# Performance work log

Measured on AMD Instinct MI355X. Metric: run time of the kernel, lower is better.

Reference implementation:

```python
import jax, jax.numpy as jnp
import numpy as np
from jax import lax

FEAT_STRIDE = 16
ANCHOR_DIMS = np.array([[64., 64.], [128., 128.], [256., 256.], [512., 512.]], np.float32)
A = ANCHOR_DIMS.shape[0]
SCALE = 1.0
PRE_NMS = 6000
POST_NMS = 300
NMS_THRESH = 0.7
MIN_SIZE = 16.0


def _anchors(H, W):
    # base anchors centered in the first feature cell, shifted over the grid
    ctr = (FEAT_STRIDE - 1.0) / 2.0
    wh = ANCHOR_DIMS * SCALE
    base = np.stack([ctr - 0.5 * (wh[:, 0] - 1), ctr - 0.5 * (wh[:, 1] - 1),
                     ctr + 0.5 * (wh[:, 0] - 1), ctr + 0.5 * (wh[:, 1] - 1)], 1)  # (A,4)
    sx = (np.arange(W) * FEAT_STRIDE).astype(np.float32)
    sy = (np.arange(H) * FEAT_STRIDE).astype(np.float32)
    gy, gx = np.meshgrid(sy, sx, indexing='ij')
    shifts = np.stack([gx.ravel(), gy.ravel(), gx.ravel(), gy.ravel()], 1)  # (H*W,4)
    return jnp.asarray((shifts[:, None, :] + base[None, :, :]).reshape(-1, 4))  # (H*W*A,4)


def _decode(anchors, deltas):
    # anchors (N,4) x1y1x2y2; deltas (B,N,4) dx,dy,dw,dh
    w = anchors[:, 2] - anchors[:, 0] + 1.0
    h = anchors[:, 3] - anchors[:, 1] + 1.0
    cx = anchors[:, 0] + 0.5 * w
    cy = anchors[:, 1] + 0.5 * h
    pcx = deltas[..., 0] * w + cx
    pcy = deltas[..., 1] * h + cy
    pw = jnp.exp(deltas[..., 2]) * w
    ph = jnp.exp(deltas[..., 3]) * h
    return jnp.stack([pcx - 0.5 * pw, pcy - 0.5 * ph, pcx + 0.5 * pw, pcy + 0.5 * ph], -1)


def _nms(boxes, scores):
    # iterative greedy NMS with fixed POST_NMS iterations (jit-friendly)
    x1, y1, x2, y2 = boxes[:, 0], boxes[:, 1], boxes[:, 2], boxes[:, 3]
    areas = (x2 - x1 + 1.0) * (y2 - y1 + 1.0)

    def step(sc, _):
        j = jnp.argmax(sc)
        xx1 = jnp.maximum(x1[j], x1); yy1 = jnp.maximum(y1[j], y1)
        xx2 = jnp.minimum(x2[j], x2); yy2 = jnp.minimum(y2[j], y2)
        inter = jnp.maximum(xx2 - xx1 + 1.0, 0.0) * jnp.maximum(yy2 - yy1 + 1.0, 0.0)
        iou = inter / (areas[j] + areas - inter)
        # iou(j,j)=1 > thresh, so the selected box suppresses itself
        return jnp.where(iou > NMS_THRESH, -jnp.inf, sc), j

    _, keep = lax.scan(step, scores, None, length=POST_NMS)
    return keep  # (POST_NMS,) int


def setup_inputs() -> dict:
    key = jax.random.key(0)
    ks = jax.random.split(key, 6)
    B = 2
    base_features = jax.random.normal(ks[0], (B, 1024, 64, 64), jnp.float32)
    image_metadata = jnp.tile(jnp.array([1024.0, 1024.0, 1.0], jnp.float32), (B, 1))
    gt_boxes = jax.random.uniform(ks[1], (B, 20, 5), jnp.float32) * 100.0
    W_conv = jax.random.normal(ks[2], (512, 1024, 3, 3), jnp.float32) * 0.01
    b_conv = jnp.zeros((512,), jnp.float32)
    W_cls = jax.random.normal(ks[3], (A, 512), jnp.float32) * 0.01
    b_cls = jnp.zeros((A,), jnp.float32)
    W_bbox = jax.random.normal(ks[4], (A * 4, 512), jnp.float32) * 0.01
    b_bbox = jnp.zeros((A * 4,), jnp.float32)
    return dict(base_features=base_features, image_metadata=image_metadata, gt_boxes=gt_boxes,
                W_conv=W_conv, b_conv=b_conv, W_cls=W_cls, b_cls=b_cls,
                W_bbox=W_bbox, b_bbox=b_bbox)


def reference(base_features, image_metadata, gt_boxes, W_conv, b_conv, W_cls, b_cls, W_bbox, b_bbox):
    B, C, H, W = base_features.shape
    # 3x3 conv + relu
    x = lax.conv_general_dilated(base_features, W_conv, (1, 1), 'SAME',
                                 dimension_numbers=('NCHW', 'OIHW', 'NCHW'))
    x = jax.nn.relu(x + b_conv[None, :, None, None])
    # 1x1 cls head, then the RPN reshape->softmax(dim=1)->reshape trick
    score = jnp.einsum('bchw,oc->bohw', x, W_cls) + b_cls[None, :, None, None]  # (B,A,H,W)
    s2 = score.reshape(B, 2, (A * H) // 2, W)
    prob = jax.nn.softmax(s2, axis=1).reshape(B, A, H, W)
    # 1x1 bbox head
    deltas = jnp.einsum('bchw,oc->bohw', x, W_bbox) + b_bbox[None, :, None, None]  # (B,4A,H,W)

    scores = prob.transpose(0, 2, 3, 1).reshape(B, -1)          # (B, H*W*A)
    d = deltas.transpose(0, 2, 3, 1).reshape(B, -1, 4)           # (B, H*W*A, 4)
    anchors = _anchors(H, W)
    props = _decode(anchors, d)                                  # (B, N, 4)
    # clip to image
    im_h = image_metadata[:, 0][:, None]
    im_w = image_metadata[:, 1][:, None]
    px1 = jnp.clip(props[..., 0], 0.0, im_w - 1.0)
    py1 = jnp.clip(props[..., 1], 0.0, im_h - 1.0)
    px2 = jnp.clip(props[..., 2], 0.0, im_w - 1.0)
    py2 = jnp.clip(props[..., 3], 0.0, im_h - 1.0)
    props = jnp.stack([px1, py1, px2, py2], -1)
    # min-size filter (mask scores instead of dynamic filtering)
    min_sz = MIN_SIZE * image_metadata[:, 2][:, None]
    keep_min = ((px2 - px1 + 1.0) >= min_sz) & ((py2 - py1 + 1.0) >= min_sz)
    scores = jnp.where(keep_min, scores, -jnp.inf)
    # pre-NMS top-k by score
    sv, si = lax.top_k(scores, PRE_NMS)
    bt = jnp.take_along_axis(props, si[..., None], axis=1)       # (B, PRE_NMS, 4)
    # NMS per image
    keep = jax.vmap(_nms)(bt, sv)                                 # (B, POST_NMS)
    boxes = jnp.take_along_axis(bt, keep[..., None], axis=1)     # (B, POST_NMS, 4)
    bidx = jnp.broadcast_to(jnp.arange(B, dtype=boxes.dtype)[:, None, None], (B, POST_NMS, 1))
    rois = jnp.concatenate([bidx, boxes], -1)                     # (B, POST_NMS, 5)
    return rois
```

## Files before the change

### kernel.cpp

```cpp
#include <hip/hip_runtime.h>
#include <stdint.h>

typedef unsigned long long ull;

#define NEGINF_ORD 0x007FFFFFu

__device__ __forceinline__ unsigned ordf(float f) {
    unsigned u = __float_as_uint(f);
    return (u & 0x80000000u) ? ~u : (u | 0x80000000u);
}

__device__ __forceinline__ void gl16(const float* g, float* l) {
    __builtin_amdgcn_global_load_lds(
        (const __attribute__((address_space(1))) unsigned*)g,
        (__attribute__((address_space(3))) unsigned*)l, 16, 0, 0);
}

__global__ __launch_bounds__(256) void zero_fill(float* __restrict__ z) {
    z[threadIdx.x] = 0.f;
}

__global__ __launch_bounds__(256) void reorder_w(const float* __restrict__ W, float* __restrict__ Wt2) {
    __shared__ float t[16][65];
    const int kb = blockIdx.x * 16;
    const int ot = blockIdx.y;
    const int tid = threadIdx.x;
#pragma unroll
    for (int r = 0; r < 4; ++r) {
        int e = tid + 256 * r;
        int o_l = e >> 4, kk = e & 15;
        t[kk][o_l] = W[(size_t)(ot * 64 + o_l) * 9216 + kb + kk];
    }
    __syncthreads();
#pragma unroll
    for (int r = 0; r < 4; ++r) {
        int e = tid + 256 * r;
        int kk = e >> 6, o_l = e & 63;
        Wt2[((size_t)ot * 9216 + kb + kk) * 64 + o_l] = t[kk][o_l];
    }
}

__global__ __launch_bounds__(256) void conv3x3_kernel(
    const float* __restrict__ Wt2, const float* __restrict__ in,
    const float* __restrict__ zerop, const float* __restrict__ bc,
    float* __restrict__ xout)
{
    __shared__ __align__(16) float Wb[2][36 * 64];
    __shared__ __align__(16) float Ib[2][4 * 4 * 64];

    const int h0 = blockIdx.x * 2;
    const int ot = blockIdx.y;
    const int b  = blockIdx.z;
    const int tid = threadIdx.x;
    const int tx = tid & 15;
    const int hloc = (tid >> 4) & 1;
    const int ty = tid >> 5;
    const int wv = tid >> 6;
    const int ln = tid & 63;
    const int w0i = tx * 4;

    const int r_ln = ln >> 4;
    const int wc_ln = (ln & 15) * 4;
    const int hin = h0 - 1 + r_ln;
    const bool hok = (hin >= 0) && (hin < 64);
    const float* isrc = in + ((size_t)(b * 1024) * 64 + (hok ? hin : 0)) * 64 + wc_ln;
    const float* zsrc = zerop + ln * 4;
    const float* wsrc = Wt2 + (size_t)ot * 9216 * 64 + ln * 4;

    auto stage = [&](int cc, int buf) {
        const float* wsB = wsrc + (size_t)cc * 36 * 64;
#pragma unroll
        for (int j = 0; j < 3; ++j) {
            int m = wv + 4 * j;
            if (m < 9)
                gl16(wsB + (size_t)m * 256, &Wb[buf][m * 256]);
        }
        const float* s = hok ? (isrc + (size_t)(cc * 4 + wv) * 4096) : zsrc;
        gl16(s, &Ib[buf][wv * 256]);
    };

    float acc[8][4], accc[8][4];
#pragma unroll
    for (int i = 0; i < 8; ++i)
#pragma unroll
        for (int j = 0; j < 4; ++j) { acc[i][j] = 0.f; accc[i][j] = 0.f; }

    stage(0, 0);
    __syncthreads();

    for (int cc = 0; cc < 256; ++cc) {
        const int buf = cc & 1;
        if (cc + 1 < 256) stage(cc + 1, buf ^ 1);

#pragma unroll
        for (int c = 0; c < 4; ++c) {
            const float* irow = &Ib[buf][c * 256];
            const float* wbase = &Wb[buf][c * 9 * 64 + ty * 8];
#pragma unroll
            for (int kh = 0; kh < 3; ++kh) {
                const float* row = irow + (hloc + kh) * 64;
                float4 v0 = *(const float4*)(row + w0i);
                float xl = (tx == 0) ? 0.f : row[w0i - 1];
                float xrr = (tx == 15) ? 0.f : row[w0i + 4];
                float xr[6];
                xr[0] = xl; xr[1] = v0.x; xr[2] = v0.y; xr[3] = v0.z; xr[4] = v0.w;
                xr[5] = xrr;
#pragma unroll
                for (int kw = 0; kw < 3; ++kw) {
                    const float* wr = wbase + (kh * 3 + kw) * 64;
                    float4 wa = *(const float4*)wr;
                    float4 wb2 = *(const float4*)(wr + 4);
#pragma unroll
                    for (int jw = 0; jw < 4; ++jw) {
                        float xv = xr[kw + jw];
                        accc[0][jw] += wa.x * xv;
                        accc[1][jw] += wa.y * xv;
                        accc[2][jw] += wa.z * xv;
                        accc[3][jw] += wa.w * xv;
                        accc[4][jw] += wb2.x * xv;
                        accc[5][jw] += wb2.y * xv;
                        accc[6][jw] += wb2.z * xv;
                        accc[7][jw] += wb2.w * xv;
                    }
                }
            }
        }
        if (cc & 1) {
#pragma unroll
            for (int i = 0; i < 8; ++i)
#pragma unroll
                for (int j = 0; j < 4; ++j) { acc[i][j] += accc[i][j]; accc[i][j] = 0.f; }
        }
        __syncthreads();
    }

    const int h = h0 + hloc;
#pragma unroll
    for (int i = 0; i < 8; ++i) {
        int o = ot * 64 + ty * 8 + i;
        float bias = bc[o];
        float4 r0;
        r0.x = fmaxf(acc[i][0] + bias, 0.f);
        r0.y = fmaxf(acc[i][1] + bias, 0.f);
        r0.z = fmaxf(acc[i][2] + bias, 0.f);
        r0.w = fmaxf(acc[i][3] + bias, 0.f);
        size_t off = (((size_t)(b * 512 + o) * 64) + h) * 64 + w0i;
        *(float4*)&xout[off] = r0;
    }
}

__global__ __launch_bounds__(256) void head_kernel(
    const float* __restrict__ x, const float* __restrict__ Wcls,
    const float* __restrict__ bcls, const float* __restrict__ Wbb,
    const float* __restrict__ bbb, const float* __restrict__ meta,
    ull* __restrict__ keys, float4* __restrict__ boxes)
{
    __shared__ __align__(16) float Wl[512 * 20];
    const int b = blockIdx.y, blk = blockIdx.x, tid = threadIdx.x;

#pragma unroll
    for (int r = 0; r < 40; ++r) {
        int L = tid + 256 * r;
        int c = L / 20, j = L - 20 * c;
        Wl[c * 20 + j] = (j < 4) ? Wcls[j * 512 + c] : Wbb[(j - 4) * 512 + c];
    }
    __syncthreads();

    const int p = blk * 256 + tid;
    const float* xb = x + (size_t)(b * 512) * 4096 + p;

    float acc[20];
#pragma unroll
    for (int j = 0; j < 20; ++j) acc[j] = 0.f;

    for (int c0 = 0; c0 < 512; c0 += 64) {
        float at[20];
#pragma unroll
        for (int j = 0; j < 20; ++j) at[j] = 0.f;
        for (int c = c0; c < c0 + 64; ++c) {
            float xv = xb[(size_t)c * 4096];
            const float4* wr = (const float4*)(Wl + c * 20);
            float4 w0 = wr[0], w1 = wr[1], w2 = wr[2], w3 = wr[3], w4 = wr[4];
            at[0] += w0.x * xv;  at[1] += w0.y * xv;  at[2] += w0.z * xv;  at[3] += w0.w * xv;
            at[4] += w1.x * xv;  at[5] += w1.y * xv;  at[6] += w1.z * xv;  at[7] += w1.w * xv;
            at[8] += w2.x * xv;  at[9] += w2.y * xv;  at[10] += w2.z * xv; at[11] += w2.w * xv;
            at[12] += w3.x * xv; at[13] += w3.y * xv; at[14] += w3.z * xv; at[15] += w3.w * xv;
            at[16] += w4.x * xv; at[17] += w4.y * xv; at[18] += w4.z * xv; at[19] += w4.w * xv;
        }
#pragma unroll
        for (int j = 0; j < 20; ++j) acc[j] += at[j];
    }

    float s[4], d[16];
#pragma unroll
    for (int j = 0; j < 4; ++j) s[j] = acc[j] + bcls[j];
#pragma unroll
    for (int j = 0; j < 16; ++j) d[j] = acc[4 + j] + bbb[j];

    float prob[4];
#pragma unroll
    for (int pr = 0; pr < 2; ++pr) {
        float m = fmaxf(s[pr], s[pr + 2]);
        float e0 = expf(s[pr] - m), e2 = expf(s[pr + 2] - m);
        float sum = e0 + e2;
        prob[pr] = e0 / sum;
        prob[pr + 2] = e2 / sum;
    }

    const float imh1 = meta[b * 3 + 0] - 1.0f;
    const float imw1 = meta[b * 3 + 1] - 1.0f;
    const float minsz = 16.0f * meta[b * 3 + 2];
    const int wp = p & 63, hp = p >> 6;
    const float cx = (float)(wp * 16 + 8), cy = (float)(hp * 16 + 8);

#pragma unroll
    for (int a = 0; a < 4; ++a) {
        float wa = (float)(64 << a);
        float pcx = d[4 * a + 0] * wa + cx;
        float pcy = d[4 * a + 1] * wa + cy;
        float pw = expf(d[4 * a + 2]) * wa;
        float ph = expf(d[4 * a + 3]) * wa;
        float x1 = pcx - 0.5f * pw, y1 = pcy - 0.5f * ph;
        float x2 = pcx + 0.5f * pw, y2 = pcy + 0.5f * ph;
        x1 = fminf(fmaxf(x1, 0.f), imw1);
        y1 = fminf(fmaxf(y1, 0.f), imh1);
        x2 = fminf(fmaxf(x2, 0.f), imw1);
        y2 = fminf(fmaxf(y2, 0.f), imh1);
        bool keep = (((x2 - x1) + 1.0f) >= minsz) && (((y2 - y1) + 1.0f) >= minsz);
        float sc = keep ? prob[a] : -__builtin_inff();
        int n = p * 4 + a;
        keys[b * 16384 + n] = ((ull)ordf(sc) << 32) | (ull)(unsigned)(16383 - n);
        float4 bx; bx.x = x1; bx.y = y1; bx.z = x2; bx.w = y2;
        boxes[b * 16384 + n] = bx;
    }
}

__global__ __launch_bounds__(512) void sort_local(ull* __restrict__ keys, int kfirst, int klast)
{
    __shared__ ull s[4096];
    const int b = blockIdx.y, chunk = blockIdx.x, tid = threadIdx.x;
    ull* g = keys + b * 16384 + chunk * 4096;
#pragma unroll
    for (int r = 0; r < 8; ++r) s[tid + 512 * r] = g[tid + 512 * r];
    __syncthreads();
    const int gbase = chunk * 4096;
    for (int k = kfirst; k <= klast; k <<= 1) {
        int j0 = (k >> 1) < 2048 ? (k >> 1) : 2048;
        for (int j = j0; j > 0; j >>= 1) {
#pragma unroll
            for (int pp = 0; pp < 4; ++pp) {
                int p = tid + 512 * pp;
                int i = ((p & ~(j - 1)) << 1) | (p & (j - 1));
                int l = i + j;
                ull a = s[i], c = s[l];
                bool up = (((gbase + i) & k) == 0);
                bool sw = up ? (a < c) : (c < a);
                if (sw) { s[i] = c; s[l] = a; }
            }
            __syncthreads();
        }
    }
#pragma unroll
    for (int r = 0; r < 8; ++r) g[tid + 512 * r] = s[tid + 512 * r];
}

__global__ __launch_bounds__(256) void sort_global_k(ull* __restrict__ keys, int k, int j)
{
    int t = blockIdx.x * 256 + threadIdx.x;
    int b = t >> 13, p = t & 8191;
    int i = ((p & ~(j - 1)) << 1) | (p & (j - 1));
    int l = i + j;
    ull* g = keys + b * 16384;
    ull a = g[i], c = g[l];
    bool up = ((i & k) == 0);
    bool sw = up ? (a < c) : (c < a);
    if (sw) { g[i] = c; g[l] = a; }
}

__global__ __launch_bounds__(256) void gather_kernel(
    const ull* __restrict__ keys, const float4* __restrict__ boxes,
    float4* __restrict__ bs, float* __restrict__ as_, ull* __restrict__ valid)
{
    const int b = blockIdx.y;
    const int i = blockIdx.x * 256 + threadIdx.x;
    bool fin = false;
    float4 box; box.x = 0.f; box.y = 0.f; box.z = 0.f; box.w = 0.f;
    float area = 1.f;
    if (i < 6000) {
        ull k = keys[b * 16384 + i];
        fin = ((unsigned)(k >> 32)) != NEGINF_ORD;
        int idx = 16383 - (int)(k & 0xFFFFFFFFull);
        box = boxes[b * 16384 + idx];
        area = ((box.z - box.x) + 1.0f) * ((box.w - box.y) + 1.0f);
    }
    bs[b * 6144 + i] = box;
    as_[b * 6144 + i] = area;
    ull m = __ballot(fin ? 1 : 0);
    if ((threadIdx.x & 63) == 0) valid[b * 96 + (i >> 6)] = m;
}

__global__ __launch_bounds__(1024) void nms_kernel(
    const float4* __restrict__ bs, const float* __restrict__ as_,
    const ull* __restrict__ valid, float* __restrict__ out)
{
    __shared__ unsigned alive[192];
    __shared__ int keepL[300];
    __shared__ int jsh;
    __shared__ int cur_sh;

    const int b = blockIdx.x, tid = threadIdx.x;

    if (tid < 96) {
        ull w = valid[b * 96 + tid];
        alive[tid * 2] = (unsigned)w;
        alive[tid * 2 + 1] = (unsigned)(w >> 32);
    }
    if (tid == 0) cur_sh = 0;
    __syncthreads();

    float4 box[6]; float area[6]; bool sf[6];
#pragma unroll
    for (int q = 0; q < 6; ++q) {
        int i = tid * 6 + q;
        box[q] = bs[b * 6144 + i];
        area[q] = as_[b * 6144 + i];
        sf[q] = !((alive[i >> 5] >> (i & 31)) & 1u);
    }
    __syncthreads();

    for (int t = 0; t < 300; ++t) {
        if (tid == 0) {
            int w = cur_sh;
            unsigned v = 0;
            while (w < 192 && (v = alive[w]) == 0u) ++w;
            int j;
            if (w < 192) {
                int bit = __ffs(v) - 1;
                j = w * 32 + bit;
                alive[w] = v & (v - 1);
            } else {
                j = 0;
            }
            cur_sh = w;
            jsh = j; keepL[t] = j;
        }
        __syncthreads();
        const int j = jsh;
        const float4 jb = bs[b * 6144 + j];
        const float ja = as_[b * 6144 + j];
#pragma unroll
        for (int q = 0; q < 6; ++q) {
            int i = tid * 6 + q;
            if (i == j) sf[q] = true;
            if (!sf[q] && i > j) {
                float xx1 = fmaxf(jb.x, box[q].x);
                float yy1 = fmaxf(jb.y, box[q].y);
                float xx2 = fminf(jb.z, box[q].z);
                float yy2 = fminf(jb.w, box[q].w);
                float iw = fmaxf((xx2 - xx1) + 1.0f, 0.f);
                float ih = fmaxf((yy2 - yy1) + 1.0f, 0.f);
                float inter = iw * ih;
                float iou = inter / ((ja + area[q]) - inter);
                if (iou > 0.7f) {
                    sf[q] = true;
                    atomicAnd(&alive[i >> 5], ~(1u << (i & 31)));
                }
            }
        }
        __syncthreads();
    }

    if (tid < 300) {
        int j = keepL[tid];
        float4 bx = bs[b * 6144 + j];
        float* o = out + (size_t)(b * 300 + tid) * 5;
        o[0] = (float)b; o[1] = bx.x; o[2] = bx.y; o[3] = bx.z; o[4] = bx.w;
    }
}

extern "C" void kernel_launch(void* const* d_in, const int* in_sizes, int n_in,
                              void* d_out, int out_size, void* d_ws, size_t ws_size,
                              hipStream_t stream) {
    const float* feat  = (const float*)d_in[0];
    const float* meta  = (const float*)d_in[1];
    const float* Wconv = (const float*)d_in[3];
    const float* bconv = (const float*)d_in[4];
    const float* Wcls  = (const float*)d_in[5];
    const float* bcls  = (const float*)d_in[6];
    const float* Wbb   = (const float*)d_in[7];
    const float* bbb   = (const float*)d_in[8];
    float* out = (float*)d_out;

    char* ws = (char*)d_ws;
    float*  x     = (float*)(ws);
    float*  Wt2   = (float*)(ws + 16777216);
    float*  zerop = (float*)(ws + 35651584);
    ull*    keys  = (ull*)(ws + 35655680);
    float4* boxes = (float4*)(ws + 35917824);
    float4* bsort = (float4*)(ws + 36966400);
    float*  asort = (float*)(ws + 37163008);
    ull*    valid = (ull*)(ws + 37212160);

    zero_fill<<<1, 256, 0, stream>>>(zerop);
    reorder_w<<<dim3(576, 8), 256, 0, stream>>>(Wconv, Wt2);
    conv3x3_kernel<<<dim3(32, 8, 2), 256, 0, stream>>>(Wt2, feat, zerop, bconv, x);
    head_kernel<<<dim3(16, 2), 256, 0, stream>>>(x, Wcls, bcls, Wbb, bbb, meta, keys, boxes);
    sort_local<<<dim3(4, 2), 512, 0, stream>>>(keys, 2, 4096);
    sort_global_k<<<64, 256, 0, stream>>>(keys, 8192, 4096);
    sort_local<<<dim3(4, 2), 512, 0, stream>>>(keys, 8192, 8192);
    sort_global_k<<<64, 256, 0, stream>>>(keys, 16384, 8192);
    sort_global_k<<<64, 256, 0, stream>>>(keys, 16384, 4096);
    sort_local<<<dim3(4, 2), 512, 0, stream>>>(keys, 16384, 16384);
    gather_kernel<<<dim3(24, 2), 256, 0, stream>>>(keys, boxes, bsort, asort, valid);
    nms_kernel<<<2, 1024, 0, stream>>>(bsort, asort, valid, out);
}
```

Measured before the change: 2.639 ms.

## Read conv weights from global via wave-uniform scalar loads, drop LDS weight staging

New measurement: 2.467 ms. -6.5%, faster.

```diff
diff --git a/kernel.cpp b/kernel.cpp
--- a/kernel.cpp
+++ b/kernel.cpp
@@ -20,63 +20,60 @@
     z[threadIdx.x] = 0.f;
 }
 
-__global__ __launch_bounds__(256) void reorder_w(const float* __restrict__ W, float* __restrict__ Wt2) {
-    __shared__ float t[16][65];
-    const int kb = blockIdx.x * 16;
-    const int ot = blockIdx.y;
+__global__ __launch_bounds__(256) void reorder_w(const float* __restrict__ W, float* __restrict__ Wt3) {
+    __shared__ float t[8][580];
+    const int cb = blockIdx.x;
+    const int wv = blockIdx.y;
+    const int ot = blockIdx.z;
     const int tid = threadIdx.x;
-#pragma unroll
-    for (int r = 0; r < 4; ++r) {
-        int e = tid + 256 * r;
-        int o_l = e >> 4, kk = e & 15;
-        t[kk][o_l] = W[(size_t)(ot * 64 + o_l) * 9216 + kb + kk];
-    }
-    __syncthreads();
-#pragma unroll
-    for (int r = 0; r < 4; ++r) {
-        int e = tid + 256 * r;
-        int kk = e >> 6, o_l = e & 63;
-        Wt2[((size_t)ot * 9216 + kb + kk) * 64 + o_l] = t[kk][o_l];
+    for (int e = tid; e < 8 * 576; e += 256) {
+        int i = e / 576, k = e - i * 576;
+        t[i][k] = W[(size_t)(ot * 32 + wv * 8 + i) * 9216 + cb * 576 + k];
+    }
+    __syncthreads();
+    for (int e = tid; e < 4608; e += 256) {
+        int cl = e / 72, r = e - cl * 72;
+        int kk = r >> 3, i = r & 7;
+        Wt3[((size_t)(ot * 1024 + cb * 64 + cl) * 4 + wv) * 72 + r] = t[i][cl * 9 + kk];
     }
 }
 
 __global__ __launch_bounds__(256) void conv3x3_kernel(
-    const float* __restrict__ Wt2, const float* __restrict__ in,
+    const float* __restrict__ Wt3, const float* __restrict__ in,
     const float* __restrict__ zerop, const float* __restrict__ bc,
     float* __restrict__ xout)
 {
-    __shared__ __align__(16) float Wb[2][36 * 64];
-    __shared__ __align__(16) float Ib[2][4 * 4 * 64];
-
-    const int h0 = blockIdx.x * 2;
+    __shared__ __align__(16) float Ib[2][4][6][64];
+
+    const int h0 = blockIdx.x * 4;
     const int ot = blockIdx.y;
     const int b  = blockIdx.z;
     const int tid = threadIdx.x;
-    const int tx = tid & 15;
-    const int hloc = (tid >> 4) & 1;
-    const int ty = tid >> 5;
     const int wv = tid >> 6;
     const int ln = tid & 63;
+    const int tx = ln & 15;
+    const int hq = ln >> 4;
     const int w0i = tx * 4;
-
-    const int r_ln = ln >> 4;
-    const int wc_ln = (ln & 15) * 4;
-    const int hin = h0 - 1 + r_ln;
-    const bool hok = (hin >= 0) && (hin < 64);
-    const float* isrc = in + ((size_t)(b * 1024) * 64 + (hok ? hin : 0)) * 64 + wc_ln;
+    const int wvu = __builtin_amdgcn_readfirstlane(wv);
+
+    const float* wsg = Wt3 + ((size_t)ot * 4096 + wvu) * 72;
     const float* zsrc = zerop + ln * 4;
-    const float* wsrc = Wt2 + (size_t)ot * 9216 * 64 + ln * 4;
 
     auto stage = [&](int cc, int buf) {
-        const float* wsB = wsrc + (size_t)cc * 36 * 64;
-#pragma unroll
-        for (int j = 0; j < 3; ++j) {
-            int m = wv + 4 * j;
-            if (m < 9)
-                gl16(wsB + (size_t)m * 256, &Wb[buf][m * 256]);
-        }
-        const float* s = hok ? (isrc + (size_t)(cc * 4 + wv) * 4096) : zsrc;
-        gl16(s, &Ib[buf][wv * 256]);
+#pragma unroll
+        for (int jj = 0; jj < 2; ++jj) {
+            int j = wv + 4 * jj;
+            if (j < 6) {
+                int r = 4 * j + hq;
+                int c = r / 6, rr = r - 6 * c;
+                int hin = h0 - 1 + rr;
+                bool ok = (hin >= 0) && (hin < 64);
+                const float* s = ok
+                    ? in + (((size_t)(b * 1024 + cc * 4 + c) * 64) + hin) * 64 + tx * 4
+                    : zsrc;
+                gl16(s, &Ib[buf][0][0][0] + j * 256);
+            }
+        }
     };
 
     float acc[8][4], accc[8][4];
@@ -93,34 +90,31 @@
         if (cc + 1 < 256) stage(cc + 1, buf ^ 1);
 
 #pragma unroll
-        for (int c = 0; c < 4; ++c) {
-            const float* irow = &Ib[buf][c * 256];
-            const float* wbase = &Wb[buf][c * 9 * 64 + ty * 8];
+        for (int ci = 0; ci < 4; ++ci) {
+            const float* wc = wsg + (size_t)(cc * 4 + ci) * 288;
 #pragma unroll
             for (int kh = 0; kh < 3; ++kh) {
-                const float* row = irow + (hloc + kh) * 64;
-                float4 v0 = *(const float4*)(row + w0i);
-                float xl = (tx == 0) ? 0.f : row[w0i - 1];
-                float xrr = (tx == 15) ? 0.f : row[w0i + 4];
+                const float* rowp = &Ib[buf][ci][hq + kh][0];
+                float4 v0 = *(const float4*)(rowp + w0i);
+                float xl = (tx == 0) ? 0.f : rowp[w0i - 1];
+                float xrr = (tx == 15) ? 0.f : rowp[w0i + 4];
                 float xr[6];
                 xr[0] = xl; xr[1] = v0.x; xr[2] = v0.y; xr[3] = v0.z; xr[4] = v0.w;
                 xr[5] = xrr;
 #pragma unroll
                 for (int kw = 0; kw < 3; ++kw) {
-                    const float* wr = wbase + (kh * 3 + kw) * 64;
-                    float4 wa = *(const float4*)wr;
-                    float4 wb2 = *(const float4*)(wr + 4);
+                    const float* w8 = wc + (kh * 3 + kw) * 8;
 #pragma unroll
                     for (int jw = 0; jw < 4; ++jw) {
                         float xv = xr[kw + jw];
-                        accc[0][jw] += wa.x * xv;
-                        accc[1][jw] += wa.y * xv;
-                        accc[2][jw] += wa.z * xv;
-                        accc[3][jw] += wa.w * xv;
-                        accc[4][jw] += wb2.x * xv;
-                        accc[5][jw] += wb2.y * xv;
-                        accc[6][jw] += wb2.z * xv;
-                        accc[7][jw] += wb2.w * xv;
+                        accc[0][jw] += w8[0] * xv;
+                        accc[1][jw] += w8[1] * xv;
+                        accc[2][jw] += w8[2] * xv;
+                        accc[3][jw] += w8[3] * xv;
+                        accc[4][jw] += w8[4] * xv;
+                        accc[5][jw] += w8[5] * xv;
+                        accc[6][jw] += w8[6] * xv;
+                        accc[7][jw] += w8[7] * xv;
                     }
                 }
             }
@@ -134,10 +128,10 @@
         __syncthreads();
     }
 
-    const int h = h0 + hloc;
+    const int h = h0 + hq;
 #pragma unroll
     for (int i = 0; i < 8; ++i) {
-        int o = ot * 64 + ty * 8 + i;
+        int o = ot * 32 + wvu * 8 + i;
         float bias = bc[o];
         float4 r0;
         r0.x = fmaxf(acc[i][0] + bias, 0.f);
@@ -402,8 +396,8 @@
     ull*    valid = (ull*)(ws + 37212160);
 
     zero_fill<<<1, 256, 0, stream>>>(zerop);
-    reorder_w<<<dim3(576, 8), 256, 0, stream>>>(Wconv, Wt2);
-    conv3x3_kernel<<<dim3(32, 8, 2), 256, 0, stream>>>(Wt2, feat, zerop, bconv, x);
+    reorder_w<<<dim3(16, 4, 16), 256, 0, stream>>>(Wconv, Wt2);
+    conv3x3_kernel<<<dim3(16, 16, 2), 256, 0, stream>>>(Wt2, feat, zerop, bconv, x);
     head_kernel<<<dim3(16, 2), 256, 0, stream>>>(x, Wcls, bcls, Wbb, bbb, meta, keys, boxes);
     sort_local<<<dim3(4, 2), 512, 0, stream>>>(keys, 2, 4096);
     sort_global_k<<<64, 256, 0, stream>>>(keys, 8192, 4096);
```
